# Kernel tuning notes

Hardware: AMD Instinct MI355X
Metric: run time of the kernel (lower is better)

## Reference

```python
import jax, jax.numpy as jnp
import numpy as np

NG, N, NFG, NFR, NFP, B = 4, 64, 1024, 256, 256, 2048
SCALE = 1.0 / float(np.sqrt(NFR + NFP))
EPS = 1e-5  # torch LayerNorm default


def setup_inputs() -> dict:
    key = jax.random.key(0)
    k = jax.random.split(key, 4)
    x = jax.random.normal(k[0], (B, N, NFG), dtype=jnp.float32)
    # per-graph params stacked over NG for vectorized computation
    Wt = jax.random.normal(k[1], (NG, NFR, NFG), dtype=jnp.float32) * 0.02
    bt = jnp.zeros((NG, NFR), dtype=jnp.float32)
    Wp = jax.random.normal(k[2], (NG, NFR, NFG), dtype=jnp.float32) * 0.02
    bp = jnp.zeros((NG, NFR), dtype=jnp.float32)
    Wg = jax.random.normal(k[3], (NG, NFG, NFG), dtype=jnp.float32) * 0.02  # [out,in]
    gamma = jnp.ones((NG, NFG), dtype=jnp.float32)
    beta = jnp.zeros((NG, NFG), dtype=jnp.float32)
    return {"x": x, "Wt": Wt, "bt": bt, "Wp": Wp, "bp": bp,
            "Wg": Wg, "gamma": gamma, "beta": beta}


def reference(x, Wt, bt, Wp, bp, Wg, gamma, beta):
    # theta/phi projections, vectorized over NG graphs: [G,B,N,R]
    theta = jnp.einsum('bnf,grf->gbnr', x, Wt) + bt[:, None, None, :]
    phi = jnp.einsum('bnf,grf->gbnr', x, Wp) + bp[:, None, None, :]
    # original computes sim=theta@phi^T then .sum(2); identical math:
    # relation[b,n] = theta[b,n] . sum_m phi[b,m]  (avoids the NxN matrix)
    phi_sum = phi.sum(axis=2)                                  # [G,B,R]
    relation = jnp.einsum('gbnr,gbr->gbn', theta, phi_sum) * SCALE
    w = jax.nn.softmax(relation, axis=2)                       # softmax over boxes N
    # attention-weighted aggregation over boxes -> [G,B,NFG]
    agg = jnp.einsum('gbn,bnf->gbf', w, x)
    # GCN linear (no bias): [G,B,NFG]
    h = jnp.einsum('gbf,gof->gbo', agg, Wg)
    # LayerNorm over feature dim, per graph
    mu = h.mean(axis=-1, keepdims=True)
    var = ((h - mu) ** 2).mean(axis=-1, keepdims=True)
    h = (h - mu) * jax.lax.rsqrt(var + EPS) * gamma[:, None, :] + beta[:, None, :]
    h = jax.nn.relu(h)
    # mean over the NG graphs; restore keepdim axis -> [B,1,NFG]
    return h.mean(axis=0)[:, None, :]
```

## Files before the change

kernel.cpp:

```cpp
#include <hip/hip_runtime.h>
#include <hip/hip_bf16.h>

typedef __attribute__((ext_vector_type(4))) float f4;
typedef __attribute__((ext_vector_type(4))) float f32x4;
typedef __attribute__((ext_vector_type(8))) short short8;
typedef __attribute__((ext_vector_type(2))) unsigned int u32x2;
typedef __attribute__((ext_vector_type(4))) unsigned int u32x4;
typedef unsigned int u32;
typedef unsigned short u16;

#define SCALE_F 0.04419417382415922f

__device__ inline u16 f2bf(float f) {
  u32 u = __float_as_uint(f);
  u32 r = u + 0x7FFFu + ((u >> 16) & 1u);
  return (u16)(r >> 16);
}
__device__ inline float bflo(u32 u) { return __uint_as_float(u << 16); }
__device__ inline float bfhi(u32 u) { return __uint_as_float(u & 0xFFFF0000u); }

__global__ __launch_bounds__(256) void k0_cvt(const float* __restrict__ src,
                                              u16* __restrict__ dst) {
  int i = blockIdx.x * 256 + threadIdx.x;
  const f4* s = (const f4*)src;
  f4 a = s[(size_t)i * 2];
  f4 b = s[(size_t)i * 2 + 1];
  u32x4 p;
  p[0] = (u32)f2bf(a[0]) | ((u32)f2bf(a[1]) << 16);
  p[1] = (u32)f2bf(a[2]) | ((u32)f2bf(a[3]) << 16);
  p[2] = (u32)f2bf(b[0]) | ((u32)f2bf(b[1]) << 16);
  p[3] = (u32)f2bf(b[2]) | ((u32)f2bf(b[3]) << 16);
  *(u32x4*)(dst + (size_t)i * 8) = p;
}

__global__ __launch_bounds__(256) void k0_wt(const float* __restrict__ Wt,
                                             u16* __restrict__ Wtt) {
  const int g = blockIdx.z;
  const int f0 = blockIdx.x * 64, r0 = blockIdx.y * 64;
  __shared__ u16 tile[64][66];
  const int t = threadIdx.x;
  const float* src = Wt + ((size_t)g * 256 + r0) * 1024 + f0;
#pragma unroll
  for (int i = 0; i < 16; ++i) {
    int idx = t + i * 256;
    int rl = idx >> 6, fl = idx & 63;
    tile[fl][rl] = f2bf(src[rl * 1024 + fl]);
  }
  __syncthreads();
  u16* dst = Wtt + ((size_t)g * 1024 + f0) * 256 + r0;
#pragma unroll
  for (int i = 0; i < 4; ++i) {
    int idx = t + i * 256;
    int fl = idx >> 4, rq = idx & 15;
    u32x2 p;
    p[0] = (u32)tile[fl][rq * 4]     | ((u32)tile[fl][rq * 4 + 1] << 16);
    p[1] = (u32)tile[fl][rq * 4 + 2] | ((u32)tile[fl][rq * 4 + 3] << 16);
    *(u32x2*)(dst + fl * 256 + rq * 4) = p;
  }
}

__global__ __launch_bounds__(256) void k1_colsum(const float* __restrict__ x,
                                                 u16* __restrict__ xs16) {
  int b = blockIdx.x, t = threadIdx.x;
  const float* xb = x + (size_t)b * (64 * 1024);
  f4 acc = {0.f, 0.f, 0.f, 0.f};
#pragma unroll 8
  for (int n = 0; n < 64; ++n)
    acc += *(const f4*)(xb + n * 1024 + t * 4);
  u32x2 p;
  p[0] = (u32)f2bf(acc[0]) | ((u32)f2bf(acc[1]) << 16);
  p[1] = (u32)f2bf(acc[2]) | ((u32)f2bf(acc[3]) << 16);
  *(u32x2*)(xs16 + (size_t)b * 1024 + t * 4) = p;
}

__global__ __launch_bounds__(256) void k2_gemm(const u16* __restrict__ A,
                                               const u16* __restrict__ Bt,
                                               const float* __restrict__ bp,
                                               u16* __restrict__ C) {
  const int n0 = blockIdx.x * 128, m0 = blockIdx.y * 128;
  __shared__ u16 Al[128 * 32];
  __shared__ u16 Bl[128 * 32];
  const int t = threadIdx.x;
  const int w = t >> 6, l = t & 63;
  const int wr = w >> 1, wc = w & 1;
  const int lr = l & 15, lh = l >> 4;
  f32x4 acc[4][4] = {};
  for (int kt = 0; kt < 1024; kt += 32) {
#pragma unroll
    for (int j = 0; j < 2; ++j) {
      int idx = t + j * 256;
      int row = idx >> 2, sl = idx & 3;
      *(u32x4*)(Al + row * 32 + sl * 8) =
          *(const u32x4*)(A + (size_t)(m0 + row) * 1024 + kt + sl * 8);
      *(u32x4*)(Bl + row * 32 + sl * 8) =
          *(const u32x4*)(Bt + (size_t)(n0 + row) * 1024 + kt + sl * 8);
    }
    __syncthreads();
    short8 af[4], bfr[4];
#pragma unroll
    for (int m = 0; m < 4; ++m)
      af[m] = *(const short8*)(Al + (wr * 64 + m * 16 + lr) * 32 + lh * 8);
#pragma unroll
    for (int n = 0; n < 4; ++n)
      bfr[n] = *(const short8*)(Bl + (wc * 64 + n * 16 + lr) * 32 + lh * 8);
#pragma unroll
    for (int m = 0; m < 4; ++m)
#pragma unroll
      for (int n = 0; n < 4; ++n)
        acc[m][n] = __builtin_amdgcn_mfma_f32_16x16x32_bf16(af[m], bfr[n],
                                                            acc[m][n], 0, 0, 0);
    __syncthreads();
  }
#pragma unroll
  for (int m = 0; m < 4; ++m)
#pragma unroll
    for (int n = 0; n < 4; ++n) {
      int col = n0 + wc * 64 + n * 16 + lr;
      float bb = 64.0f * bp[col];
#pragma unroll
      for (int j = 0; j < 4; ++j)
        C[(size_t)(m0 + wr * 64 + m * 16 + lh * 4 + j) * 1024 + col] =
            f2bf(acc[m][n][j] + bb);
    }
}

__global__ __launch_bounds__(256) void k3_gemm(const u16* __restrict__ A,
                                               const u16* __restrict__ Btt,
                                               float* __restrict__ V) {
  const int g = blockIdx.z;
  const int n0 = blockIdx.x * 128, m0 = blockIdx.y * 128;
  const u16* Bg = Btt + (size_t)g * 1024 * 256;
  __shared__ u16 Al[128 * 32];
  __shared__ u16 Bl[128 * 32];
  const int t = threadIdx.x;
  const int w = t >> 6, l = t & 63;
  const int wr = w >> 1, wc = w & 1;
  const int lr = l & 15, lh = l >> 4;
  f32x4 acc[4][4] = {};
  for (int kt = 0; kt < 256; kt += 32) {
#pragma unroll
    for (int j = 0; j < 2; ++j) {
      int idx = t + j * 256;
      int row = idx >> 2, sl = idx & 3;
      *(u32x4*)(Al + row * 32 + sl * 8) =
          *(const u32x4*)(A + (size_t)(m0 + row) * 1024 + g * 256 + kt + sl * 8);
      *(u32x4*)(Bl + row * 32 + sl * 8) =
          *(const u32x4*)(Bg + (size_t)(n0 + row) * 256 + kt + sl * 8);
    }
    __syncthreads();
    short8 af[4], bfr[4];
#pragma unroll
    for (int m = 0; m < 4; ++m)
      af[m] = *(const short8*)(Al + (wr * 64 + m * 16 + lr) * 32 + lh * 8);
#pragma unroll
    for (int n = 0; n < 4; ++n)
      bfr[n] = *(const short8*)(Bl + (wc * 64 + n * 16 + lr) * 32 + lh * 8);
#pragma unroll
    for (int m = 0; m < 4; ++m)
#pragma unroll
      for (int n = 0; n < 4; ++n)
        acc[m][n] = __builtin_amdgcn_mfma_f32_16x16x32_bf16(af[m], bfr[n],
                                                            acc[m][n], 0, 0, 0);
    __syncthreads();
  }
  float* Vg = V + (size_t)g * 2048 * 1024;
#pragma unroll
  for (int m = 0; m < 4; ++m)
#pragma unroll
    for (int n = 0; n < 4; ++n)
#pragma unroll
      for (int j = 0; j < 4; ++j)
        Vg[(size_t)(m0 + wr * 64 + m * 16 + lh * 4 + j) * 1024 +
           (n0 + wc * 64 + n * 16 + lr)] = acc[m][n][j];
}

#define K4_LDS (131072 + 16384 + 2048 + 1024)
__global__ __launch_bounds__(512) void k4_fused(const float* __restrict__ x,
                                                const float* __restrict__ V,
                                                u16* __restrict__ aggb) {
  extern __shared__ char sm[];
  char* xl = sm;
  float* vl = (float*)(sm + 131072);
  float* relp = (float*)(sm + 131072 + 16384);
  float* wsm = relp + 512;
  const int t = threadIdx.x;
  const int b = blockIdx.x;
  const float* xb = x + (size_t)b * (64 * 1024);

#pragma unroll 4
  for (int i = 0; i < 32; ++i) {
    int idx = t + i * 512;
    int row = idx >> 8, col4 = idx & 255;
    f4 a = *(const f4*)(xb + row * 1024 + col4 * 4);
    u32 p0 = (u32)f2bf(a[0]) | ((u32)f2bf(a[1]) << 16);
    u32 p1 = (u32)f2bf(a[2]) | ((u32)f2bf(a[3]) << 16);
    int slot = col4 >> 1, half = col4 & 1;
    char* dst = xl + row * 2048 + ((slot ^ (row & 7)) << 4) + half * 8;
    ((u32*)dst)[0] = p0;
    ((u32*)dst)[1] = p1;
  }
#pragma unroll
  for (int i = 0; i < 2; ++i) {
    int idx = t + i * 512;
    int g = idx >> 8, q = idx & 255;
    *(f4*)(vl + g * 1024 + q * 4) =
        *(const f4*)(V + ((size_t)g * 2048 + b) * 1024 + q * 4);
  }
  __syncthreads();

  {
    const int h = t >> 8, g = (t >> 6) & 3, n = t & 63;
    const char* xrow = xl + n * 2048;
    const float* vg = vl + g * 1024;
    const int sw = n & 7;
    float racc = 0.f;
#pragma unroll 4
    for (int f0 = h * 512; f0 < h * 512 + 512; f0 += 8) {
      u32x4 xp = *(const u32x4*)(xrow + (((f0 >> 3) ^ sw) << 4));
      f4 v0 = *(const f4*)(vg + f0);
      f4 v1 = *(const f4*)(vg + f0 + 4);
      racc = fmaf(bflo(xp[0]), v0[0], racc);
      racc = fmaf(bfhi(xp[0]), v0[1], racc);
      racc = fmaf(bflo(xp[1]), v0[2], racc);
      racc = fmaf(bfhi(xp[1]), v0[3], racc);
      racc = fmaf(bflo(xp[2]), v1[0], racc);
      racc = fmaf(bfhi(xp[2]), v1[1], racc);
      racc = fmaf(bflo(xp[3]), v1[2], racc);
      racc = fmaf(bfhi(xp[3]), v1[3], racc);
    }
    relp[t] = racc;
  }
  __syncthreads();

  if (t < 256) {
    float rel = (relp[t] + relp[t + 256]) * SCALE_F;
    float mx = rel;
#pragma unroll
    for (int o = 32; o > 0; o >>= 1) mx = fmaxf(mx, __shfl_xor(mx, o, 64));
    float e = __expf(rel - mx);
    float s = e;
#pragma unroll
    for (int o = 32; o > 0; o >>= 1) s += __shfl_xor(s, o, 64);
    wsm[t] = e / s;
  }
  __syncthreads();

  {
    const int g = t >> 7, fb = (t & 127) << 3;
    const float* wg = wsm + g * 64;
    const int baseslot = fb >> 3;
    float a0 = 0, a1 = 0, a2 = 0, a3 = 0, a4 = 0, a5 = 0, a6 = 0, a7 = 0;
#pragma unroll 8
    for (int n = 0; n < 64; ++n) {
      float w = wg[n];
      u32x4 xp = *(const u32x4*)(xl + n * 2048 + ((baseslot ^ (n & 7)) << 4));
      a0 = fmaf(bflo(xp[0]), w, a0);
      a1 = fmaf(bfhi(xp[0]), w, a1);
      a2 = fmaf(bflo(xp[1]), w, a2);
      a3 = fmaf(bfhi(xp[1]), w, a3);
      a4 = fmaf(bflo(xp[2]), w, a4);
      a5 = fmaf(bfhi(xp[2]), w, a5);
      a6 = fmaf(bflo(xp[3]), w, a6);
      a7 = fmaf(bfhi(xp[3]), w, a7);
    }
    u32x4 p;
    p[0] = (u32)f2bf(a0) | ((u32)f2bf(a1) << 16);
    p[1] = (u32)f2bf(a2) | ((u32)f2bf(a3) << 16);
    p[2] = (u32)f2bf(a4) | ((u32)f2bf(a5) << 16);
    p[3] = (u32)f2bf(a6) | ((u32)f2bf(a7) << 16);
    *(u32x4*)(aggb + ((size_t)g * 2048 + b) * 1024 + fb) = p;
  }
}

__global__ __launch_bounds__(256) void k5_gemm(const u16* __restrict__ Ab,
                                               const u16* __restrict__ Bb,
                                               float* __restrict__ H) {
  const int g = blockIdx.z;
  const int n0 = blockIdx.x * 128, m0 = blockIdx.y * 128;
  const u16* A = Ab + (size_t)g * 2048 * 1024;
  const u16* Bt = Bb + (size_t)g * 1024 * 1024;
  __shared__ u16 Al[128 * 32];
  __shared__ u16 Bl[128 * 32];
  const int t = threadIdx.x;
  const int w = t >> 6, l = t & 63;
  const int wr = w >> 1, wc = w & 1;
  const int lr = l & 15, lh = l >> 4;
  f32x4 acc[4][4] = {};
  for (int kt = 0; kt < 1024; kt += 32) {
#pragma unroll
    for (int j = 0; j < 2; ++j) {
      int idx = t + j * 256;
      int row = idx >> 2, sl = idx & 3;
      *(u32x4*)(Al + row * 32 + sl * 8) =
          *(const u32x4*)(A + (size_t)(m0 + row) * 1024 + kt + sl * 8);
      *(u32x4*)(Bl + row * 32 + sl * 8) =
          *(const u32x4*)(Bt + (size_t)(n0 + row) * 1024 + kt + sl * 8);
    }
    __syncthreads();
    short8 af[4], bfr[4];
#pragma unroll
    for (int m = 0; m < 4; ++m)
      af[m] = *(const short8*)(Al + (wr * 64 + m * 16 + lr) * 32 + lh * 8);
#pragma unroll
    for (int n = 0; n < 4; ++n)
      bfr[n] = *(const short8*)(Bl + (wc * 64 + n * 16 + lr) * 32 + lh * 8);
#pragma unroll
    for (int m = 0; m < 4; ++m)
#pragma unroll
      for (int n = 0; n < 4; ++n)
        acc[m][n] = __builtin_amdgcn_mfma_f32_16x16x32_bf16(af[m], bfr[n],
                                                            acc[m][n], 0, 0, 0);
    __syncthreads();
  }
  float* Hg = H + (size_t)g * 2048 * 1024;
#pragma unroll
  for (int m = 0; m < 4; ++m)
#pragma unroll
    for (int n = 0; n < 4; ++n)
#pragma unroll
      for (int j = 0; j < 4; ++j)
        Hg[(size_t)(m0 + wr * 64 + m * 16 + lh * 4 + j) * 1024 +
           (n0 + wc * 64 + n * 16 + lr)] = acc[m][n][j];
}

__global__ __launch_bounds__(256) void k6_ln(const float* __restrict__ H,
                                             const float* __restrict__ gamma,
                                             const float* __restrict__ beta,
                                             float* __restrict__ out) {
  const int b = blockIdx.x, t = threadIdx.x;
  const int w = t >> 6, lane = t & 63;
  __shared__ float red[8];
  f4 acc = {0.f, 0.f, 0.f, 0.f};
  for (int g = 0; g < 4; ++g) {
    f4 hv = *(const f4*)(H + ((size_t)g * 2048 + b) * 1024 + t * 4);
    float s = hv[0] + hv[1] + hv[2] + hv[3];
    float q = hv[0] * hv[0] + hv[1] * hv[1] + hv[2] * hv[2] + hv[3] * hv[3];
#pragma unroll
    for (int o = 32; o > 0; o >>= 1) {
      s += __shfl_xor(s, o, 64);
      q += __shfl_xor(q, o, 64);
    }
    if (lane == 0) { red[w] = s; red[4 + w] = q; }
    __syncthreads();
    s = red[0] + red[1] + red[2] + red[3];
    q = red[4] + red[5] + red[6] + red[7];
    float mean = s * (1.f / 1024.f);
    float var = q * (1.f / 1024.f) - mean * mean;
    float rstd = rsqrtf(var + 1e-5f);
    f4 gm = *(const f4*)(gamma + g * 1024 + t * 4);
    f4 bt = *(const f4*)(beta + g * 1024 + t * 4);
#pragma unroll
    for (int j = 0; j < 4; ++j) {
      float val = (hv[j] - mean) * rstd * gm[j] + bt[j];
      acc[j] += fmaxf(val, 0.f);
    }
    __syncthreads();
  }
  acc *= 0.25f;
  *(f4*)(out + (size_t)b * 1024 + t * 4) = acc;
}

extern "C" void kernel_launch(void* const* d_in, const int* in_sizes, int n_in,
                              void* d_out, int out_size, void* d_ws, size_t ws_size,
                              hipStream_t stream) {
  const float* x     = (const float*)d_in[0];
  const float* Wt    = (const float*)d_in[1];
  const float* Wp    = (const float*)d_in[3];
  const float* bp    = (const float*)d_in[4];
  const float* Wg    = (const float*)d_in[5];
  const float* gamma = (const float*)d_in[6];
  const float* beta  = (const float*)d_in[7];
  float* out = (float*)d_out;

  char* ws = (char*)d_ws;
  u16*   xs16 = (u16*)(ws);
  u16*   ps16 = (u16*)(ws + (4u << 20));
  u16*   wpb  = (u16*)(ws + (8u << 20));
  u16*   wtb  = (u16*)(ws + (10u << 20));
  u16*   wgb  = (u16*)(ws + (12u << 20));
  float* v    = (float*)(ws + (20u << 20));
  float* h    = (float*)(ws + (20u << 20));
  u16*   aggb = (u16*)(ws + (52u << 20));

  hipFuncSetAttribute((const void*)k4_fused,
                      hipFuncAttributeMaxDynamicSharedMemorySize, K4_LDS);

  k0_cvt<<<2048, 256, 0, stream>>>(Wg, wgb);
  k0_cvt<<<512, 256, 0, stream>>>(Wp, wpb);
  k0_wt<<<dim3(16, 4, 4), 256, 0, stream>>>(Wt, wtb);
  k1_colsum<<<2048, 256, 0, stream>>>(x, xs16);
  k2_gemm<<<dim3(8, 16), 256, 0, stream>>>(xs16, wpb, bp, ps16);
  k3_gemm<<<dim3(8, 16, 4), 256, 0, stream>>>(ps16, wtb, v);
  k4_fused<<<2048, 512, K4_LDS, stream>>>(x, v, aggb);
  k5_gemm<<<dim3(8, 16, 4), 256, 0, stream>>>(aggb, wgb, h);
  k6_ln<<<2048, 256, 0, stream>>>(h, gamma, beta, out);
}
```

Baseline: 383.0 us.

## Use direct global-to-LDS loads in GEMMs and pipeline x loading in fused attention kernel

The three GEMM kernels now stage tiles with global_load_lds, moving data straight into shared memory instead of through registers. The fused attention kernel runs 1024 threads and loads x in two halves held in registers. The relation dot products for the first 32 boxes are computed while the second half of x is still being fetched, which is meant to hide HBM latency behind compute. The cost is higher register pressure and a kernel that relies on hand-placed waitcnt and barrier instructions.

```diff
diff --git a/kernel.cpp b/kernel.cpp
--- a/kernel.cpp
+++ b/kernel.cpp
@@ -18,6 +18,11 @@
 }
 __device__ inline float bflo(u32 u) { return __uint_as_float(u << 16); }
 __device__ inline float bfhi(u32 u) { return __uint_as_float(u & 0xFFFF0000u); }
+
+#define GLD16(gsrc, ldst)                                                     \
+  __builtin_amdgcn_global_load_lds(                                           \
+      (const __attribute__((address_space(1))) void*)(gsrc),                  \
+      (__attribute__((address_space(3))) void*)(ldst), 16, 0, 0)
 
 __global__ __launch_bounds__(256) void k0_cvt(const float* __restrict__ src,
                                               u16* __restrict__ dst) {
@@ -90,10 +95,8 @@
     for (int j = 0; j < 2; ++j) {
       int idx = t + j * 256;
       int row = idx >> 2, sl = idx & 3;
-      *(u32x4*)(Al + row * 32 + sl * 8) =
-          *(const u32x4*)(A + (size_t)(m0 + row) * 1024 + kt + sl * 8);
-      *(u32x4*)(Bl + row * 32 + sl * 8) =
-          *(const u32x4*)(Bt + (size_t)(n0 + row) * 1024 + kt + sl * 8);
+      GLD16(A + (size_t)(m0 + row) * 1024 + kt + sl * 8, Al + idx * 8);
+      GLD16(Bt + (size_t)(n0 + row) * 1024 + kt + sl * 8, Bl + idx * 8);
     }
     __syncthreads();
     short8 af[4], bfr[4];
@@ -142,10 +145,8 @@
     for (int j = 0; j < 2; ++j) {
       int idx = t + j * 256;
       int row = idx >> 2, sl = idx & 3;
-      *(u32x4*)(Al + row * 32 + sl * 8) =
-          *(const u32x4*)(A + (size_t)(m0 + row) * 1024 + g * 256 + kt + sl * 8);
-      *(u32x4*)(Bl + row * 32 + sl * 8) =
-          *(const u32x4*)(Bg + (size_t)(n0 + row) * 256 + kt + sl * 8);
+      GLD16(A + (size_t)(m0 + row) * 1024 + g * 256 + kt + sl * 8, Al + idx * 8);
+      GLD16(Bg + (size_t)(n0 + row) * 256 + kt + sl * 8, Bl + idx * 8);
     }
     __syncthreads();
     short8 af[4], bfr[4];
@@ -174,51 +175,59 @@
            (n0 + wc * 64 + n * 16 + lr)] = acc[m][n][j];
 }
 
-#define K4_LDS (131072 + 16384 + 2048 + 1024)
-__global__ __launch_bounds__(512) void k4_fused(const float* __restrict__ x,
-                                                const float* __restrict__ V,
-                                                u16* __restrict__ aggb) {
+#define K4_LDS (131072 + 16384 + 8192 + 1024)
+__global__ __launch_bounds__(1024) void k4_fused(const float* __restrict__ x,
+                                                 const float* __restrict__ V,
+                                                 u16* __restrict__ aggb) {
   extern __shared__ char sm[];
   char* xl = sm;
   float* vl = (float*)(sm + 131072);
   float* relp = (float*)(sm + 131072 + 16384);
-  float* wsm = relp + 512;
+  float* wsm = (float*)(sm + 131072 + 16384 + 8192);
   const int t = threadIdx.x;
   const int b = blockIdx.x;
-  const float* xb = x + (size_t)b * (64 * 1024);
-
-#pragma unroll 4
-  for (int i = 0; i < 32; ++i) {
-    int idx = t + i * 512;
+  const float* xb = x + (size_t)b * 65536;
+
+  f4 va = *(const f4*)(V + ((size_t)(t >> 8) * 2048 + b) * 1024 + (t & 255) * 4);
+  f4 xr[8];
+#pragma unroll
+  for (int i = 0; i < 8; ++i) {
+    int idx = i * 1024 + t;
+    xr[i] = *(const f4*)(xb + (idx >> 8) * 1024 + (idx & 255) * 4);
+  }
+  *(f4*)(vl + t * 4) = va;
+#pragma unroll
+  for (int i = 0; i < 8; ++i) {
+    int idx = i * 1024 + t;
     int row = idx >> 8, col4 = idx & 255;
-    f4 a = *(const f4*)(xb + row * 1024 + col4 * 4);
-    u32 p0 = (u32)f2bf(a[0]) | ((u32)f2bf(a[1]) << 16);
-    u32 p1 = (u32)f2bf(a[2]) | ((u32)f2bf(a[3]) << 16);
+    u32 p0 = (u32)f2bf(xr[i][0]) | ((u32)f2bf(xr[i][1]) << 16);
+    u32 p1 = (u32)f2bf(xr[i][2]) | ((u32)f2bf(xr[i][3]) << 16);
     int slot = col4 >> 1, half = col4 & 1;
     char* dst = xl + row * 2048 + ((slot ^ (row & 7)) << 4) + half * 8;
     ((u32*)dst)[0] = p0;
     ((u32*)dst)[1] = p1;
   }
-#pragma unroll
-  for (int i = 0; i < 2; ++i) {
-    int idx = t + i * 512;
-    int g = idx >> 8, q = idx & 255;
-    *(f4*)(vl + g * 1024 + q * 4) =
-        *(const f4*)(V + ((size_t)g * 2048 + b) * 1024 + q * 4);
-  }
-  __syncthreads();
+  f4 xr2[8];
+#pragma unroll
+  for (int i = 0; i < 8; ++i) {
+    int idx = 8192 + i * 1024 + t;
+    xr2[i] = *(const f4*)(xb + (idx >> 8) * 1024 + (idx & 255) * 4);
+  }
+  asm volatile("s_waitcnt lgkmcnt(0)" ::: "memory");
+  __builtin_amdgcn_s_barrier();
 
   {
-    const int h = t >> 8, g = (t >> 6) & 3, n = t & 63;
+    const int h = t >> 7, g = (t >> 5) & 3, n = t & 31;
     const char* xrow = xl + n * 2048;
-    const float* vg = vl + g * 1024;
+    const float* vg = vl + g * 1024 + h * 128;
     const int sw = n & 7;
     float racc = 0.f;
-#pragma unroll 4
-    for (int f0 = h * 512; f0 < h * 512 + 512; f0 += 8) {
-      u32x4 xp = *(const u32x4*)(xrow + (((f0 >> 3) ^ sw) << 4));
-      f4 v0 = *(const f4*)(vg + f0);
-      f4 v1 = *(const f4*)(vg + f0 + 4);
+#pragma unroll
+    for (int f8 = 0; f8 < 16; ++f8) {
+      int slot = h * 16 + f8;
+      u32x4 xp = *(const u32x4*)(xrow + ((slot ^ sw) << 4));
+      f4 v0 = *(const f4*)(vg + f8 * 8);
+      f4 v1 = *(const f4*)(vg + f8 * 8 + 4);
       racc = fmaf(bflo(xp[0]), v0[0], racc);
       racc = fmaf(bfhi(xp[0]), v0[1], racc);
       racc = fmaf(bflo(xp[1]), v0[2], racc);
@@ -230,10 +239,53 @@
     }
     relp[t] = racc;
   }
+#pragma unroll
+  for (int i = 0; i < 8; ++i) {
+    int idx = 8192 + i * 1024 + t;
+    int row = idx >> 8, col4 = idx & 255;
+    u32 p0 = (u32)f2bf(xr2[i][0]) | ((u32)f2bf(xr2[i][1]) << 16);
+    u32 p1 = (u32)f2bf(xr2[i][2]) | ((u32)f2bf(xr2[i][3]) << 16);
+    int slot = col4 >> 1, half = col4 & 1;
+    char* dst = xl + row * 2048 + ((slot ^ (row & 7)) << 4) + half * 8;
+    ((u32*)dst)[0] = p0;
+    ((u32*)dst)[1] = p1;
+  }
+  asm volatile("s_waitcnt lgkmcnt(0)" ::: "memory");
+  __builtin_amdgcn_s_barrier();
+
+  {
+    const int h = t >> 7, g = (t >> 5) & 3, n = 32 + (t & 31);
+    const char* xrow = xl + n * 2048;
+    const float* vg = vl + g * 1024 + h * 128;
+    const int sw = n & 7;
+    float racc = 0.f;
+#pragma unroll
+    for (int f8 = 0; f8 < 16; ++f8) {
+      int slot = h * 16 + f8;
+      u32x4 xp = *(const u32x4*)(xrow + ((slot ^ sw) << 4));
+      f4 v0 = *(const f4*)(vg + f8 * 8);
+      f4 v1 = *(const f4*)(vg + f8 * 8 + 4);
+      racc = fmaf(bflo(xp[0]), v0[0], racc);
+      racc = fmaf(bfhi(xp[0]), v0[1], racc);
+      racc = fmaf(bflo(xp[1]), v0[2], racc);
+      racc = fmaf(bfhi(xp[1]), v0[3], racc);
+      racc = fmaf(bflo(xp[2]), v1[0], racc);
+      racc = fmaf(bfhi(xp[2]), v1[1], racc);
+      racc = fmaf(bflo(xp[3]), v1[2], racc);
+      racc = fmaf(bfhi(xp[3]), v1[3], racc);
+    }
+    relp[1024 + t] = racc;
+  }
   __syncthreads();
 
   if (t < 256) {
-    float rel = (relp[t] + relp[t + 256]) * SCALE_F;
+    const int g = t >> 6, n = t & 63;
+    const float* base = (n < 32) ? (relp + g * 32 + (n & 31))
+                                 : (relp + 1024 + g * 32 + (n & 31));
+    float rel = 0.f;
+#pragma unroll
+    for (int h = 0; h < 8; ++h) rel += base[h * 128];
+    rel *= SCALE_F;
     float mx = rel;
 #pragma unroll
     for (int o = 32; o > 0; o >>= 1) mx = fmaxf(mx, __shfl_xor(mx, o, 64));
@@ -246,29 +298,23 @@
   __syncthreads();
 
   {
-    const int g = t >> 7, fb = (t & 127) << 3;
+    const int g = t >> 8, fb4 = t & 255;
     const float* wg = wsm + g * 64;
-    const int baseslot = fb >> 3;
-    float a0 = 0, a1 = 0, a2 = 0, a3 = 0, a4 = 0, a5 = 0, a6 = 0, a7 = 0;
+    const int slot = fb4 >> 1, half = fb4 & 1;
+    float a0 = 0, a1 = 0, a2 = 0, a3 = 0;
 #pragma unroll 8
     for (int n = 0; n < 64; ++n) {
       float w = wg[n];
-      u32x4 xp = *(const u32x4*)(xl + n * 2048 + ((baseslot ^ (n & 7)) << 4));
+      u32x2 xp = *(const u32x2*)(xl + n * 2048 + ((slot ^ (n & 7)) << 4) + half * 8);
       a0 = fmaf(bflo(xp[0]), w, a0);
       a1 = fmaf(bfhi(xp[0]), w, a1);
       a2 = fmaf(bflo(xp[1]), w, a2);
       a3 = fmaf(bfhi(xp[1]), w, a3);
-      a4 = fmaf(bflo(xp[2]), w, a4);
-      a5 = fmaf(bfhi(xp[2]), w, a5);
-      a6 = fmaf(bflo(xp[3]), w, a6);
-      a7 = fmaf(bfhi(xp[3]), w, a7);
-    }
-    u32x4 p;
+    }
+    u32x2 p;
     p[0] = (u32)f2bf(a0) | ((u32)f2bf(a1) << 16);
     p[1] = (u32)f2bf(a2) | ((u32)f2bf(a3) << 16);
-    p[2] = (u32)f2bf(a4) | ((u32)f2bf(a5) << 16);
-    p[3] = (u32)f2bf(a6) | ((u32)f2bf(a7) << 16);
-    *(u32x4*)(aggb + ((size_t)g * 2048 + b) * 1024 + fb) = p;
+    *(u32x2*)(aggb + ((size_t)g * 2048 + b) * 1024 + fb4 * 4) = p;
   }
 }
 
@@ -291,10 +337,8 @@
     for (int j = 0; j < 2; ++j) {
       int idx = t + j * 256;
       int row = idx >> 2, sl = idx & 3;
-      *(u32x4*)(Al + row * 32 + sl * 8) =
-          *(const u32x4*)(A + (size_t)(m0 + row) * 1024 + kt + sl * 8);
-      *(u32x4*)(Bl + row * 32 + sl * 8) =
-          *(const u32x4*)(Bt + (size_t)(n0 + row) * 1024 + kt + sl * 8);
+      GLD16(A + (size_t)(m0 + row) * 1024 + kt + sl * 8, Al + idx * 8);
+      GLD16(Bt + (size_t)(n0 + row) * 1024 + kt + sl * 8, Bl + idx * 8);
     }
     __syncthreads();
     short8 af[4], bfr[4];
@@ -391,7 +435,7 @@
   k1_colsum<<<2048, 256, 0, stream>>>(x, xs16);
   k2_gemm<<<dim3(8, 16), 256, 0, stream>>>(xs16, wpb, bp, ps16);
   k3_gemm<<<dim3(8, 16, 4), 256, 0, stream>>>(ps16, wtb, v);
-  k4_fused<<<2048, 512, K4_LDS, stream>>>(x, v, aggb);
+  k4_fused<<<2048, 1024, K4_LDS, stream>>>(x, v, aggb);
   k5_gemm<<<dim3(8, 16, 4), 256, 0, stream>>>(aggb, wgb, h);
   k6_ln<<<2048, 256, 0, stream>>>(h, gamma, beta, out);
 }
```

Measured after the change: 358.8 us. -6.3%, faster.
